# Performance work log

Hardware: AMD Instinct MI355X
Metric: run time of the kernel (lower is better)

## Reference

```python
import jax, jax.numpy as jnp
import numpy as np

D_MODEL = 1024
N_HEADS = 16
D_HEAD = D_MODEL // N_HEADS
BATCH = 2
SEQ = 2048


def spectral_linear(x, basis, scales):
    # (x @ U) * s @ U^T ; basis is a fixed (non-learned) square matrix
    return ((x @ basis) * scales) @ basis.T


def setup_inputs() -> dict:
    key = jax.random.key(0)
    ks = jax.random.split(key, 3)
    x = jax.random.normal(ks[0], (BATCH, SEQ, D_MODEL), dtype=jnp.float32)
    # orthonormal-ish spectral basis (random Gaussian scaled keeps values sane)
    basis = jax.random.normal(ks[1], (D_MODEL, D_MODEL), dtype=jnp.float32) / np.sqrt(D_MODEL)
    route_bias = jax.random.normal(ks[2], (N_HEADS, SEQ, SEQ), dtype=jnp.float32) * 0.02
    ones = jnp.ones((D_MODEL,), dtype=jnp.float32)
    return {
        "x": x,
        "basis": basis,
        "scale_q": ones,
        "scale_k": ones,
        "scale_v": ones,
        "scale_o": ones,
        "route_bias": route_bias,
    }


def reference(x, basis, scale_q, scale_k, scale_v, scale_o, route_bias):
    bsz, seq_len, _ = x.shape

    def split_heads(t):  # [b,s,d] -> [b,h,s,dh]
        return t.reshape(bsz, seq_len, N_HEADS, D_HEAD).transpose(0, 2, 1, 3)

    q = split_heads(spectral_linear(x, basis, scale_q))
    k = split_heads(spectral_linear(x, basis, scale_k))
    v = split_heads(spectral_linear(x, basis, scale_v))

    scores = jnp.einsum("bhqd,bhkd->bhqk", q, k) / np.sqrt(D_HEAD).astype(np.float32)
    scores = scores + route_bias[None, :, :seq_len, :seq_len]
    causal = jnp.triu(jnp.ones((seq_len, seq_len), dtype=bool), k=1)
    scores = jnp.where(causal[None, None], -jnp.inf, scores)
    attn = jax.nn.softmax(scores, axis=-1)
    out = jnp.einsum("bhqk,bhkd->bhqd", attn, v)
    out = out.transpose(0, 2, 1, 3).reshape(bsz, seq_len, D_MODEL)
    return spectral_linear(out, basis, scale_o)
```

## Files before the change

### kernel.cpp

```cpp
#include <hip/hip_runtime.h>
#include <stdint.h>

#define AS1 __attribute__((address_space(1)))
#define AS3 __attribute__((address_space(3)))

typedef __bf16 bf16x8 __attribute__((ext_vector_type(8)));
typedef float f32x4 __attribute__((ext_vector_type(4)));

#if defined(__has_builtin)
#if __has_builtin(__builtin_amdgcn_global_load_lds)
#define USE_GLL 1
#else
#define USE_GLL 0
#endif
#else
#define USE_GLL 0
#endif

static __device__ __forceinline__ unsigned short f2bf(float f) {
    union { float f; uint32_t u; } v; v.f = f;
    uint32_t u = v.u + 0x7fffu + ((v.u >> 16) & 1u);
    return (unsigned short)(u >> 16);
}

__global__ void k_f32_to_bf16(const float* __restrict__ in, unsigned short* __restrict__ out, int n) {
    int idx = (blockIdx.x * 256 + threadIdx.x) * 4;
    if (idx >= n) return;
    float4 v = *(const float4*)(in + idx);
    unsigned short r[4] = { f2bf(v.x), f2bf(v.y), f2bf(v.z), f2bf(v.w) };
    *(uint2*)(out + idx) = *(const uint2*)r;
}

__global__ void k_transpose_bf16(const float* __restrict__ basis, unsigned short* __restrict__ bt) {
    int idx = blockIdx.x * 256 + threadIdx.x;
    int n = idx >> 10, k = idx & 1023;
    bt[idx] = f2bf(basis[(size_t)k * 1024 + n]);
}

__global__ void k_make_scaled(const float* __restrict__ basis,
                              const float* __restrict__ sq, const float* __restrict__ sk,
                              const float* __restrict__ sv, const float* __restrict__ so,
                              unsigned short* __restrict__ Bq, unsigned short* __restrict__ Bk,
                              unsigned short* __restrict__ Bv, unsigned short* __restrict__ Bo) {
    int idx = blockIdx.x * 256 + threadIdx.x;
    int k = idx & 1023;
    float b = basis[idx];
    Bq[idx] = f2bf(b * sq[k]);
    Bk[idx] = f2bf(b * sk[k]);
    Bv[idx] = f2bf(b * sv[k]);
    Bo[idx] = f2bf(b * so[k]);
}

__global__ void k_transpose_v(const unsigned short* __restrict__ vsb, unsigned short* __restrict__ vtb) {
    __shared__ __align__(16) unsigned short t[128 * 72];
    const int sc = blockIdx.x;
    const int bh = blockIdx.y;
    const int tid = threadIdx.x;
    #pragma unroll
    for (int rep = 0; rep < 4; ++rep) {
        int idx = rep * 256 + tid;
        int s = idx >> 3, part = idx & 7;
        *(uint4*)(t + s * 72 + part * 8) =
            *(const uint4*)(vsb + ((size_t)bh * 2048 + sc * 128 + s) * 64 + part * 8);
    }
    __syncthreads();
    #pragma unroll
    for (int rep = 0; rep < 4; ++rep) {
        int idx = rep * 256 + tid;
        int d = idx >> 4, pc = idx & 15;
        unsigned short tmp[8];
        #pragma unroll
        for (int j = 0; j < 8; ++j) tmp[j] = t[(pc * 8 + j) * 72 + d];
        *(uint4*)(vtb + ((size_t)bh * 64 + d) * 2048 + sc * 128 + pc * 8) = *(const uint4*)tmp;
    }
}

#define BK 32

__global__ __launch_bounds__(256, 2)
void k_gemm_qkv(const unsigned short* __restrict__ A,
                const unsigned short* __restrict__ B,
                unsigned short* __restrict__ qkv,
                int M, int N, int K)
{
    __shared__ __align__(16) unsigned short As[128 * BK];
    __shared__ __align__(16) unsigned short Bs[128 * BK];

    const int tid  = threadIdx.x;
    const int lane = tid & 63;
    const int w    = tid >> 6;
    const int wm   = w & 1;
    const int wn   = w >> 1;
    const int bm   = blockIdx.y;
    const int bn   = blockIdx.x;
    const int fm   = lane & 15;
    const int quad = lane >> 4;
    const int fk   = quad * 8;
    const int srow = lane >> 2;
    const int spart= lane & 3;

    f32x4 zero4 = {0.f, 0.f, 0.f, 0.f};
    f32x4 acc[4][4];
    #pragma unroll
    for (int i = 0; i < 4; ++i)
        #pragma unroll
        for (int j = 0; j < 4; ++j) acc[i][j] = zero4;

    for (int k0 = 0; k0 < K; k0 += BK) {
        #pragma unroll
        for (int t = 0; t < 2; ++t) {
            int row = w * 32 + t * 16 + srow;
            const unsigned short* ga = A + (size_t)(bm * 128 + row) * K + k0 + spart * 8;
            const unsigned short* gb = B + (size_t)(bn * 128 + row) * K + k0 + spart * 8;
#if USE_GLL
            __builtin_amdgcn_global_load_lds((const void AS1*)ga, (void AS3*)(As + w * 1024 + t * 512), 16, 0, 0);
            __builtin_amdgcn_global_load_lds((const void AS1*)gb, (void AS3*)(Bs + w * 1024 + t * 512), 16, 0, 0);
#else
            *(uint4*)(As + w * 1024 + t * 512 + lane * 8) = *(const uint4*)ga;
            *(uint4*)(Bs + w * 1024 + t * 512 + lane * 8) = *(const uint4*)gb;
#endif
        }
        __syncthreads();
        bf16x8 af[4], bfr[4];
        #pragma unroll
        for (int i = 0; i < 4; ++i) af[i] = *(const bf16x8*)(As + (wm * 64 + i * 16 + fm) * BK + fk);
        #pragma unroll
        for (int j = 0; j < 4; ++j) bfr[j] = *(const bf16x8*)(Bs + (wn * 64 + j * 16 + fm) * BK + fk);
        #pragma unroll
        for (int i = 0; i < 4; ++i)
            #pragma unroll
            for (int j = 0; j < 4; ++j)
                acc[i][j] = __builtin_amdgcn_mfma_f32_16x16x32_bf16(af[i], bfr[j], acc[i][j], 0, 0, 0);
        __syncthreads();
    }

    #pragma unroll
    for (int i = 0; i < 4; ++i)
        #pragma unroll
        for (int j = 0; j < 4; ++j)
            #pragma unroll
            for (int r = 0; r < 4; ++r) {
                int row = bm * 128 + wm * 64 + i * 16 + quad * 4 + r;
                int col = bn * 128 + wn * 64 + j * 16 + fm;
                int sec = col >> 10, cc = col & 1023;
                int bb = row >> 11, s = row & 2047;
                int hh = cc >> 6,  d = cc & 63;
                qkv[((size_t)sec << 22) + (((size_t)(bb * 16 + hh)) * 2048 + s) * 64 + d] = f2bf(acc[i][j][r]);
            }
}

template<int EPI>
__global__ __launch_bounds__(256, 2)
void k_gemm_n64(const unsigned short* __restrict__ A,
                const unsigned short* __restrict__ B,
                void* __restrict__ Cout,
                int M, int N, int K)
{
    __shared__ __align__(16) unsigned short As[128 * BK];
    __shared__ __align__(16) unsigned short Bs[64 * BK];

    const int tid  = threadIdx.x;
    const int lane = tid & 63;
    const int w    = tid >> 6;
    const int wm   = w & 1;
    const int wn   = w >> 1;
    const int bm   = blockIdx.y;
    const int bn   = blockIdx.x;
    const int fm   = lane & 15;
    const int quad = lane >> 4;
    const int fk   = quad * 8;
    const int srow = lane >> 2;
    const int spart= lane & 3;

    f32x4 zero4 = {0.f, 0.f, 0.f, 0.f};
    f32x4 acc[4][2];
    #pragma unroll
    for (int i = 0; i < 4; ++i)
        #pragma unroll
        for (int j = 0; j < 2; ++j) acc[i][j] = zero4;

    for (int k0 = 0; k0 < K; k0 += BK) {
        #pragma unroll
        for (int t = 0; t < 2; ++t) {
            int row = w * 32 + t * 16 + srow;
            const unsigned short* ga = A + (size_t)(bm * 128 + row) * K + k0 + spart * 8;
#if USE_GLL
            __builtin_amdgcn_global_load_lds((const void AS1*)ga, (void AS3*)(As + w * 1024 + t * 512), 16, 0, 0);
#else
            *(uint4*)(As + w * 1024 + t * 512 + lane * 8) = *(const uint4*)ga;
#endif
        }
        {
            const unsigned short* gb = B + (size_t)(bn * 64 + w * 16 + srow) * K + k0 + spart * 8;
#if USE_GLL
            __builtin_amdgcn_global_load_lds((const void AS1*)gb, (void AS3*)(Bs + w * 512), 16, 0, 0);
#else
            *(uint4*)(Bs + w * 512 + lane * 8) = *(const uint4*)gb;
#endif
        }
        __syncthreads();
        bf16x8 af[4], bfr[2];
        #pragma unroll
        for (int i = 0; i < 4; ++i) af[i] = *(const bf16x8*)(As + (wm * 64 + i * 16 + fm) * BK + fk);
        #pragma unroll
        for (int j = 0; j < 2; ++j) bfr[j] = *(const bf16x8*)(Bs + (wn * 32 + j * 16 + fm) * BK + fk);
        #pragma unroll
        for (int i = 0; i < 4; ++i)
            #pragma unroll
            for (int j = 0; j < 2; ++j)
                acc[i][j] = __builtin_amdgcn_mfma_f32_16x16x32_bf16(af[i], bfr[j], acc[i][j], 0, 0, 0);
        __syncthreads();
    }

    #pragma unroll
    for (int i = 0; i < 4; ++i)
        #pragma unroll
        for (int j = 0; j < 2; ++j)
            #pragma unroll
            for (int r = 0; r < 4; ++r) {
                int row = bm * 128 + wm * 64 + i * 16 + quad * 4 + r;
                int col = bn * 64 + wn * 32 + j * 16 + fm;
                if (EPI == 0) ((unsigned short*)Cout)[(size_t)row * N + col] = f2bf(acc[i][j][r]);
                else          ((float*)Cout)[(size_t)row * N + col] = acc[i][j][r];
            }
}

__global__ __launch_bounds__(256, 4)
void k_attn(const unsigned short* __restrict__ qs, const unsigned short* __restrict__ ks,
            const unsigned short* __restrict__ vt, const float* __restrict__ bias,
            unsigned short* __restrict__ out)
{
    const int qt = blockIdx.x;
    const int bh = blockIdx.y;
    const int h  = bh & 15;
    const int b  = bh >> 4;
    const size_t rowbase = (size_t)bh * 2048;

    const int tid  = threadIdx.x;
    const int lane = tid & 63;
    const int w    = tid >> 6;
    const int fm   = lane & 15;
    const int quad = lane >> 4;
    const int fk   = quad * 8;

    __shared__ __align__(16) unsigned short Ks[64 * 72];
    __shared__ __align__(16) unsigned short Vt[64 * 72];
    __shared__ __align__(16) unsigned short Ps[4][16 * 72];

    const int q0 = qt * 64 + w * 16;

    bf16x8 qf[2];
    #pragma unroll
    for (int c = 0; c < 2; ++c)
        qf[c] = *(const bf16x8*)(qs + (rowbase + q0 + fm) * 64 + c * 32 + fk);

    f32x4 zero4 = {0.f, 0.f, 0.f, 0.f};
    f32x4 oacc[4];
    float lsum[4];
    #pragma unroll
    for (int jd = 0; jd < 4; ++jd) oacc[jd] = zero4;
    #pragma unroll
    for (int r = 0; r < 4; ++r) lsum[r] = 0.f;

    const int nkt = qt + 1;
    for (int kt = 0; kt < nkt; ++kt) {
        float bb[4][4];
        #pragma unroll
        for (int jn = 0; jn < 4; ++jn)
            #pragma unroll
            for (int r = 0; r < 4; ++r)
                bb[jn][r] = bias[((size_t)h * 2048 + q0 + quad * 4 + r) * 2048
                                 + kt * 64 + jn * 16 + fm];

        #pragma unroll
        for (int rep = 0; rep < 2; ++rep) {
            int idx  = rep * 256 + tid;
            int row  = idx >> 3;
            int part = idx & 7;
            *(uint4*)(Ks + row * 72 + part * 8) =
                *(const uint4*)(ks + (rowbase + kt * 64 + row) * 64 + part * 8);
            *(uint4*)(Vt + row * 72 + part * 8) =
                *(const uint4*)(vt + ((size_t)bh * 64 + row) * 2048 + kt * 64 + part * 8);
        }
        __syncthreads();

        f32x4 sacc[4];
        #pragma unroll
        for (int jn = 0; jn < 4; ++jn) sacc[jn] = zero4;
        bf16x8 kb[4][2];
        #pragma unroll
        for (int jn = 0; jn < 4; ++jn)
            #pragma unroll
            for (int c = 0; c < 2; ++c)
                kb[jn][c] = *(const bf16x8*)(Ks + (jn * 16 + fm) * 72 + c * 32 + fk);
        #pragma unroll
        for (int jn = 0; jn < 4; ++jn)
            #pragma unroll
            for (int c = 0; c < 2; ++c)
                sacc[jn] = __builtin_amdgcn_mfma_f32_16x16x32_bf16(qf[c], kb[jn][c], sacc[jn], 0, 0, 0);

        #pragma unroll
        for (int jn = 0; jn < 4; ++jn)
            #pragma unroll
            for (int r = 0; r < 4; ++r) {
                int row = q0 + quad * 4 + r;
                int col = kt * 64 + jn * 16 + fm;
                float p = exp2f(sacc[jn][r] * 0.18033688f + bb[jn][r] * 1.44269504f);
                p = (col > row) ? 0.f : p;
                lsum[r] += p;
                Ps[w][(quad * 4 + r) * 72 + jn * 16 + fm] = f2bf(p);
            }

        bf16x8 vf[4][2], pf[2];
        #pragma unroll
        for (int jd = 0; jd < 4; ++jd)
            #pragma unroll
            for (int c = 0; c < 2; ++c)
                vf[jd][c] = *(const bf16x8*)(Vt + (jd * 16 + fm) * 72 + c * 32 + fk);
        #pragma unroll
        for (int c = 0; c < 2; ++c)
            pf[c] = *(const bf16x8*)(Ps[w] + fm * 72 + c * 32 + fk);
        #pragma unroll
        for (int jd = 0; jd < 4; ++jd)
            #pragma unroll
            for (int c = 0; c < 2; ++c)
                oacc[jd] = __builtin_amdgcn_mfma_f32_16x16x32_bf16(pf[c], vf[jd][c], oacc[jd], 0, 0, 0);

        __syncthreads();
    }

    #pragma unroll
    for (int r = 0; r < 4; ++r) {
        float l = lsum[r];
        #pragma unroll
        for (int off = 1; off < 16; off <<= 1) l += __shfl_xor(l, off, 64);
        lsum[r] = 1.f / l;
    }

    #pragma unroll
    for (int jd = 0; jd < 4; ++jd)
        #pragma unroll
        for (int r = 0; r < 4; ++r) {
            int row = q0 + quad * 4 + r;
            int d   = jd * 16 + fm;
            out[((size_t)b * 2048 + row) * 1024 + h * 64 + d] = f2bf(oacc[jd][r] * lsum[r]);
        }
}

extern "C" void kernel_launch(void* const* d_in, const int* in_sizes, int n_in,
                              void* d_out, int out_size, void* d_ws, size_t ws_size,
                              hipStream_t stream) {
    (void)in_sizes; (void)n_in; (void)out_size; (void)ws_size;
    const float* x     = (const float*)d_in[0];
    const float* basis = (const float*)d_in[1];
    const float* sq    = (const float*)d_in[2];
    const float* sk    = (const float*)d_in[3];
    const float* sv    = (const float*)d_in[4];
    const float* so    = (const float*)d_in[5];
    const float* bias  = (const float*)d_in[6];
    float* out = (float*)d_out;

    char* ws = (char*)d_ws;
    size_t off = 0;
    auto alloc = [&](size_t bytes) { void* p = ws + off; off += bytes; return p; };
    unsigned short* x_bf  = (unsigned short*)alloc((size_t)8 << 20);
    unsigned short* BT    = (unsigned short*)alloc((size_t)2 << 20);
    unsigned short* Bq    = (unsigned short*)alloc((size_t)2 << 20);
    unsigned short* Bk    = (unsigned short*)alloc((size_t)2 << 20);
    unsigned short* Bv    = (unsigned short*)alloc((size_t)2 << 20);
    unsigned short* Bo    = (unsigned short*)alloc((size_t)2 << 20);
    unsigned short* xb    = (unsigned short*)alloc((size_t)8 << 20);
    unsigned short* qkvb  = (unsigned short*)alloc((size_t)24 << 20);
    unsigned short* vtb   = (unsigned short*)alloc((size_t)8 << 20);
    unsigned short* attno = (unsigned short*)alloc((size_t)8 << 20);
    unsigned short* y     = (unsigned short*)alloc((size_t)8 << 20);

    unsigned short* qsb = qkvb;
    unsigned short* ksb = qkvb + ((size_t)1 << 22);
    unsigned short* vsb = qkvb + ((size_t)2 << 22);

    k_f32_to_bf16<<<4096, 256, 0, stream>>>(x, x_bf, 4096 * 1024);
    k_transpose_bf16<<<4096, 256, 0, stream>>>(basis, BT);
    k_make_scaled<<<4096, 256, 0, stream>>>(basis, sq, sk, sv, so, Bq, Bk, Bv, Bo);

    dim3 blk(256);
    k_gemm_n64<0><<<dim3(16, 32), blk, 0, stream>>>(x_bf, BT, xb, 4096, 1024, 1024);
    k_gemm_qkv<<<dim3(24, 32), blk, 0, stream>>>(xb, Bq, qkvb, 4096, 3072, 1024);
    k_transpose_v<<<dim3(16, 32), blk, 0, stream>>>(vsb, vtb);
    k_attn<<<dim3(32, 32), blk, 0, stream>>>(qsb, ksb, vtb, bias, attno);
    k_gemm_n64<0><<<dim3(16, 32), blk, 0, stream>>>(attno, BT, y, 4096, 1024, 1024);
    k_gemm_n64<2><<<dim3(16, 32), blk, 0, stream>>>(y, Bo, out, 4096, 1024, 1024);
}
```

Baseline: 542.0 us.

## Precompute fused spectral weight matrices to eliminate per-token basis GEMMs

Folds the two-step spectral projection (x@U)*s@U^T into a single precomputed weight W=U·diag(s)·U^T for q/k/v/o, built by one GEMM over the stacked scaled bases. The token-side path then runs one QKV GEMM and one output GEMM, dropping two token GEMMs and the basis transpose kernel. It adds one weight-building GEMM per call, and rounding the combined weight to bf16 changes numerical error characteristics.

```diff
diff --git a/kernel.cpp b/kernel.cpp
--- a/kernel.cpp
+++ b/kernel.cpp
@@ -31,17 +31,12 @@
     *(uint2*)(out + idx) = *(const uint2*)r;
 }
 
-__global__ void k_transpose_bf16(const float* __restrict__ basis, unsigned short* __restrict__ bt) {
-    int idx = blockIdx.x * 256 + threadIdx.x;
-    int n = idx >> 10, k = idx & 1023;
-    bt[idx] = f2bf(basis[(size_t)k * 1024 + n]);
-}
-
 __global__ void k_make_scaled(const float* __restrict__ basis,
                               const float* __restrict__ sq, const float* __restrict__ sk,
                               const float* __restrict__ sv, const float* __restrict__ so,
                               unsigned short* __restrict__ Bq, unsigned short* __restrict__ Bk,
-                              unsigned short* __restrict__ Bv, unsigned short* __restrict__ Bo) {
+                              unsigned short* __restrict__ Bv, unsigned short* __restrict__ Bo,
+                              unsigned short* __restrict__ Ub) {
     int idx = blockIdx.x * 256 + threadIdx.x;
     int k = idx & 1023;
     float b = basis[idx];
@@ -49,6 +44,7 @@
     Bk[idx] = f2bf(b * sk[k]);
     Bv[idx] = f2bf(b * sv[k]);
     Bo[idx] = f2bf(b * so[k]);
+    Ub[idx] = f2bf(b);
 }
 
 __global__ void k_transpose_v(const unsigned short* __restrict__ vsb, unsigned short* __restrict__ vtb) {
@@ -364,30 +360,29 @@
     size_t off = 0;
     auto alloc = [&](size_t bytes) { void* p = ws + off; off += bytes; return p; };
     unsigned short* x_bf  = (unsigned short*)alloc((size_t)8 << 20);
-    unsigned short* BT    = (unsigned short*)alloc((size_t)2 << 20);
-    unsigned short* Bq    = (unsigned short*)alloc((size_t)2 << 20);
-    unsigned short* Bk    = (unsigned short*)alloc((size_t)2 << 20);
-    unsigned short* Bv    = (unsigned short*)alloc((size_t)2 << 20);
-    unsigned short* Bo    = (unsigned short*)alloc((size_t)2 << 20);
-    unsigned short* xb    = (unsigned short*)alloc((size_t)8 << 20);
+    unsigned short* Acat  = (unsigned short*)alloc((size_t)8 << 20);
+    unsigned short* Ub    = (unsigned short*)alloc((size_t)2 << 20);
+    unsigned short* Wall  = (unsigned short*)alloc((size_t)8 << 20);
     unsigned short* qkvb  = (unsigned short*)alloc((size_t)24 << 20);
     unsigned short* vtb   = (unsigned short*)alloc((size_t)8 << 20);
     unsigned short* attno = (unsigned short*)alloc((size_t)8 << 20);
-    unsigned short* y     = (unsigned short*)alloc((size_t)8 << 20);
-
+
+    unsigned short* Bq  = Acat;
+    unsigned short* Bk  = Acat + ((size_t)1 << 20);
+    unsigned short* Bv  = Acat + ((size_t)2 << 20);
+    unsigned short* Bo  = Acat + ((size_t)3 << 20);
     unsigned short* qsb = qkvb;
     unsigned short* ksb = qkvb + ((size_t)1 << 22);
     unsigned short* vsb = qkvb + ((size_t)2 << 22);
+    unsigned short* Wo  = Wall + (size_t)3 * 1024 * 1024;
 
     k_f32_to_bf16<<<4096, 256, 0, stream>>>(x, x_bf, 4096 * 1024);
-    k_transpose_bf16<<<4096, 256, 0, stream>>>(basis, BT);
-    k_make_scaled<<<4096, 256, 0, stream>>>(basis, sq, sk, sv, so, Bq, Bk, Bv, Bo);
+    k_make_scaled<<<4096, 256, 0, stream>>>(basis, sq, sk, sv, so, Bq, Bk, Bv, Bo, Ub);
 
     dim3 blk(256);
-    k_gemm_n64<0><<<dim3(16, 32), blk, 0, stream>>>(x_bf, BT, xb, 4096, 1024, 1024);
-    k_gemm_qkv<<<dim3(24, 32), blk, 0, stream>>>(xb, Bq, qkvb, 4096, 3072, 1024);
+    k_gemm_n64<0><<<dim3(16, 32), blk, 0, stream>>>(Acat, Ub, Wall, 4096, 1024, 1024);
+    k_gemm_qkv<<<dim3(24, 32), blk, 0, stream>>>(x_bf, Wall, qkvb, 4096, 3072, 1024);
     k_transpose_v<<<dim3(16, 32), blk, 0, stream>>>(vsb, vtb);
     k_attn<<<dim3(32, 32), blk, 0, stream>>>(qsb, ksb, vtb, bias, attno);
-    k_gemm_n64<0><<<dim3(16, 32), blk, 0, stream>>>(attno, BT, y, 4096, 1024, 1024);
-    k_gemm_n64<2><<<dim3(16, 32), blk, 0, stream>>>(y, Bo, out, 4096, 1024, 1024);
-}
+    k_gemm_n64<2><<<dim3(16, 32), blk, 0, stream>>>(attno, Wo, out, 4096, 1024, 1024);
+}
```

Result: faster. 516.8 us (-4.7%).
